# Kernel tuning notes

Hardware: AMD Instinct MI355X
Metric: run time of the kernel (lower is better)

Reference implementation:

```python
import jax, jax.numpy as jnp
import numpy as np

N_NODES = 50000
N_EDGES = 800000
IN_DIM = 64
HID_DIM = 64
OUT_DIM = 16
N_RELS = 16
N_BASES = 4


def setup_inputs() -> dict:
    key = jax.random.key(0)
    ks = jax.random.split(key, 11)
    feats = jax.random.normal(ks[0], (N_NODES, IN_DIM), dtype=jnp.float32)
    src = jax.random.randint(ks[1], (N_EDGES,), 0, N_NODES, dtype=jnp.int32)
    dst = jax.random.randint(ks[2], (N_EDGES,), 0, N_NODES, dtype=jnp.int32)
    edge_type = jax.random.randint(ks[3], (N_EDGES,), 0, N_RELS, dtype=jnp.int32)
    edge_norm = jax.random.uniform(ks[4], (N_EDGES,), dtype=jnp.float32)
    # basis-decomposed relation weights: W[r] = sum_b coef[r,b] * bases[b]
    bases1 = jax.random.normal(ks[5], (N_BASES, IN_DIM, HID_DIM), dtype=jnp.float32) * (1.0 / np.sqrt(IN_DIM))
    coef1 = jax.random.normal(ks[6], (N_RELS, N_BASES), dtype=jnp.float32)
    bias1 = jnp.zeros((HID_DIM,), dtype=jnp.float32)
    bases2 = jax.random.normal(ks[7], (N_BASES, HID_DIM, OUT_DIM), dtype=jnp.float32) * (1.0 / np.sqrt(HID_DIM))
    coef2 = jax.random.normal(ks[8], (N_RELS, N_BASES), dtype=jnp.float32)
    bias2 = jnp.zeros((OUT_DIM,), dtype=jnp.float32)
    return {"feats": feats, "src": src, "dst": dst, "edge_type": edge_type,
            "edge_norm": edge_norm, "bases1": bases1, "coef1": coef1, "bias1": bias1,
            "bases2": bases2, "coef2": coef2, "bias2": bias2}


def _rel_graph_conv(x, src, dst, edge_type, edge_norm, bases, coef, bias):
    """One RelGraphConv layer (basis decomposition, low-mem: gather coef, not W)."""
    xs = x[src]                                   # [E, in]  gather source feats
    t = jnp.einsum('ei,bio->ebo', xs, bases)      # [E, B, out] per-basis transform
    c = coef[edge_type]                            # [E, B]   per-edge relation coefs
    msg = jnp.einsum('eb,ebo->eo', c, t)          # [E, out]
    msg = msg * edge_norm[:, None]                # apply edge norm
    h = jax.ops.segment_sum(msg, dst, num_segments=N_NODES)  # scatter-add by dst
    return jax.nn.relu(h + bias)                  # bias + activation (dropout=0, eval)


def reference(feats, src, dst, edge_type, edge_norm, bases1, coef1, bias1, bases2, coef2, bias2):
    h = _rel_graph_conv(feats, src, dst, edge_type, edge_norm, bases1, coef1, bias1)
    h = _rel_graph_conv(h, src, dst, edge_type, edge_norm, bases2, coef2, bias2)
    return h
```

## Files before the change

### kernel.cpp

```cpp
#include <hip/hip_runtime.h>

#define N_NODES 50000
#define N_EDGES 800000

typedef __attribute__((ext_vector_type(8))) short bf16x8;
typedef __attribute__((ext_vector_type(4))) float f32x4;

__device__ __forceinline__ unsigned bf16rne(float x) {
  unsigned u = __float_as_uint(x);
  return (u + 0x7FFFu + ((u >> 16) & 1u)) >> 16;
}
__device__ __forceinline__ unsigned packbf2(float a, float b) {
  return bf16rne(a) | (bf16rne(b) << 16);
}
__device__ __forceinline__ float bflo(unsigned u) { return __uint_as_float(u << 16); }
__device__ __forceinline__ float bfhi(unsigned u) { return __uint_as_float(u & 0xFFFF0000u); }

__global__ __launch_bounds__(256) void k_pack(
    const float4* __restrict__ feats4, uint2* __restrict__ xbf,
    const float* __restrict__ bases1, const float* __restrict__ bases2,
    unsigned short* __restrict__ b1T, unsigned short* __restrict__ b2p) {
  if (blockIdx.x < 3125) {
    const int i = blockIdx.x * 256 + threadIdx.x;
    float4 v = feats4[i];
    xbf[i] = make_uint2(packbf2(v.x, v.y), packbf2(v.z, v.w));
  } else {
    for (int idx = threadIdx.x; idx < 64 * 256; idx += 256) {
      int o = idx >> 8, q = idx & 255;
      b1T[idx] = (unsigned short)bf16rne(bases1[q * 64 + o]);
    }
    for (int idx = threadIdx.x; idx < 64 * 64; idx += 256) {
      int j = idx >> 6, k = idx & 63;
      int o = j >> 2, b = j & 3;
      b2p[idx] = (unsigned short)bf16rne(bases2[b * 1024 + k * 16 + o]);
    }
  }
}

#define G_HIST 64
#define CHUNK (N_EDGES / G_HIST)
#define NSLICE 4
#define HBINS (N_NODES / NSLICE)

__global__ __launch_bounds__(512) void k_hist(
    const int* __restrict__ dst, unsigned char* __restrict__ rank,
    unsigned short* __restrict__ bh) {
  __shared__ int hist[HBINS];
  const int c = blockIdx.x & (G_HIST - 1);
  const int p = blockIdx.x >> 6;
  const int e0 = c * CHUNK;
  const int lo = p * HBINS;
  for (int i = threadIdx.x; i < HBINS; i += 512) hist[i] = 0;
  __syncthreads();
  for (int i = threadIdx.x; i < CHUNK; i += 512) {
    const int d = dst[e0 + i] - lo;
    if ((unsigned)d < (unsigned)HBINS)
      rank[e0 + i] = (unsigned char)atomicAdd(&hist[d], 1);
  }
  __syncthreads();
  for (int i = threadIdx.x; i < HBINS; i += 512)
    bh[(size_t)c * N_NODES + lo + i] = (unsigned short)hist[i];
}

#define NB 512
__global__ __launch_bounds__(512) void k_scan1(
    unsigned short* __restrict__ bh,
    int* __restrict__ rowp, int* __restrict__ bsum) {
  __shared__ unsigned short tile[G_HIST][NB];
  __shared__ int wsum[8];
  const int tid = threadIdx.x;
  const int n0 = blockIdx.x * NB;
  for (int idx = tid; idx < G_HIST * (NB / 4); idx += 512) {
    const int c = idx >> 7, j = idx & 127;
    const int nloc = 4 * j;
    uint2 u = make_uint2(0u, 0u);
    if (n0 + nloc < N_NODES)
      u = *(const uint2*)(bh + (size_t)c * N_NODES + n0 + nloc);
    *(uint2*)&tile[c][nloc] = u;
  }
  __syncthreads();
  int s = 0;
  for (int c = 0; c < G_HIST; ++c) {
    const int cnt = tile[c][tid];
    tile[c][tid] = (unsigned short)s;
    s += cnt;
  }
  __syncthreads();
  for (int idx = tid; idx < G_HIST * (NB / 4); idx += 512) {
    const int c = idx >> 7, j = idx & 127;
    const int nloc = 4 * j;
    if (n0 + nloc < N_NODES)
      *(uint2*)(bh + (size_t)c * N_NODES + n0 + nloc) = *(uint2*)&tile[c][nloc];
  }
  const int lane = tid & 63, wid = tid >> 6;
  int v = (n0 + tid < N_NODES) ? s : 0;
  int incl = v;
#pragma unroll
  for (int off = 1; off < 64; off <<= 1) {
    int t = __shfl_up(incl, off, 64);
    if (lane >= off) incl += t;
  }
  if (lane == 63) wsum[wid] = incl;
  __syncthreads();
  if (tid < 8) {
    int wi = wsum[tid];
#pragma unroll
    for (int off = 1; off < 8; off <<= 1) {
      int t = __shfl_up(wi, off, 64);
      if (lane >= off) wi += t;
    }
    wsum[tid] = wi;
  }
  __syncthreads();
  int woff = (wid > 0) ? wsum[wid - 1] : 0;
  int incl_all = incl + woff;
  if (n0 + tid < N_NODES) rowp[n0 + tid + 1] = incl_all;
  if (tid == NB - 1) bsum[blockIdx.x] = incl_all;
}

__global__ __launch_bounds__(512) void k_scan3(int* __restrict__ rowp,
                                               const int* __restrict__ bsum) {
  __shared__ int s_off;
  const int tid = threadIdx.x;
  if (tid < 64) {
    int v = 0;
    for (int b = tid; b < (int)blockIdx.x; b += 64) v += bsum[b];
#pragma unroll
    for (int off = 32; off >= 1; off >>= 1) v += __shfl_down(v, off, 64);
    if (tid == 0) s_off = v;
  }
  __syncthreads();
  const int i = blockIdx.x * NB + tid;
  if (i < N_NODES) rowp[i + 1] += s_off;
  if (i == 0) rowp[0] = 0;
}

__global__ __launch_bounds__(256) void k_scatter(
    const int* __restrict__ src, const int* __restrict__ dst,
    const int* __restrict__ ety, const float* __restrict__ enorm,
    const int* __restrict__ rowp, const unsigned char* __restrict__ rank,
    const unsigned short* __restrict__ bh, unsigned* __restrict__ s_edge) {
  int e = blockIdx.x * 256 + threadIdx.x;
  if (e >= N_EDGES) return;
  const int d = dst[e];
  const int b = e / CHUNK;
  const int pos = rowp[d] + (int)bh[(size_t)b * N_NODES + d] + (int)rank[e];
  unsigned nq = (unsigned)(enorm[e] * 4096.f + 0.5f);
  nq = nq > 4095u ? 4095u : nq;
  s_edge[pos] = (unsigned)src[e] | ((unsigned)ety[e] << 16) | (nq << 20);
}

#define NMSCALE (1.f / 4096.f)

#define ROWB 264
__device__ __forceinline__ void gather_node(
    const int* __restrict__ rowp, const unsigned* __restrict__ s_edge,
    const uint2* __restrict__ xv, const float4* __restrict__ coefLDS,
    unsigned short* __restrict__ uA,
    int node, int m, int lane) {
  const int eslot = lane >> 4, ch4 = lane & 15;
  const int beg = rowp[node], end = rowp[node + 1];
  const int qlen = (end - beg + 3) >> 2;
  int p = beg + eslot * qlen;
  const int pend = min(p + qlen, end);
  float4 a0 = {0, 0, 0, 0}, a1 = {0, 0, 0, 0}, a2 = {0, 0, 0, 0}, a3 = {0, 0, 0, 0};
  for (; p < pend; p += 4) {
    const int nb = pend - p;
    unsigned rec[4];
#pragma unroll
    for (int t = 0; t < 4; ++t) rec[t] = (t < nb) ? s_edge[p + t] : 0u;
    uint2 xp[4];
#pragma unroll
    for (int t = 0; t < 4; ++t) xp[t] = xv[(rec[t] & 0xFFFF) * 16 + ch4];
#pragma unroll
    for (int t = 0; t < 4; ++t) {
      const float nm = (float)(rec[t] >> 20) * NMSCALE;
      const float4 c = coefLDS[(rec[t] >> 16) & 15];
      const float w0 = nm * c.x, w1 = nm * c.y, w2 = nm * c.z, w3 = nm * c.w;
      const float x0 = bflo(xp[t].x), x1 = bfhi(xp[t].x);
      const float x2 = bflo(xp[t].y), x3 = bfhi(xp[t].y);
      a0.x += w0 * x0; a0.y += w0 * x1; a0.z += w0 * x2; a0.w += w0 * x3;
      a1.x += w1 * x0; a1.y += w1 * x1; a1.z += w1 * x2; a1.w += w1 * x3;
      a2.x += w2 * x0; a2.y += w2 * x1; a2.z += w2 * x2; a2.w += w2 * x3;
      a3.x += w3 * x0; a3.y += w3 * x1; a3.z += w3 * x2; a3.w += w3 * x3;
    }
  }
#define RED1(x) x += __shfl_down(x, 32, 64)
  RED1(a0.x); RED1(a0.y); RED1(a0.z); RED1(a0.w);
  RED1(a1.x); RED1(a1.y); RED1(a1.z); RED1(a1.w);
  RED1(a2.x); RED1(a2.y); RED1(a2.z); RED1(a2.w);
  RED1(a3.x); RED1(a3.y); RED1(a3.z); RED1(a3.w);
#undef RED1
  if (eslot < 2) {
    unsigned short* row = uA + (eslot * 16 + m) * ROWB + 4 * ch4;
    *(uint2*)(row + 0 * 64) = make_uint2(packbf2(a0.x, a0.y), packbf2(a0.z, a0.w));
    *(uint2*)(row + 1 * 64) = make_uint2(packbf2(a1.x, a1.y), packbf2(a1.z, a1.w));
    *(uint2*)(row + 2 * 64) = make_uint2(packbf2(a2.x, a2.y), packbf2(a2.z, a2.w));
    *(uint2*)(row + 3 * 64) = make_uint2(packbf2(a3.x, a3.y), packbf2(a3.z, a3.w));
  }
}

__global__ __launch_bounds__(256) void k_l1_fused(
    const int* __restrict__ rowp, const unsigned* __restrict__ s_edge,
    const uint2* __restrict__ xbf, const float* __restrict__ coef1,
    const unsigned short* __restrict__ b1T,
    const float* __restrict__ bias1,
    const unsigned short* __restrict__ b2p,
    uint2* __restrict__ y2bf) {
  __shared__ __align__(16) unsigned short uA[2 * 16 * ROWB];
  __shared__ float coefs[64];
  __shared__ float cmat[16 * 68];
  const int wid = threadIdx.x >> 6, lane = threadIdx.x & 63;
  if (threadIdx.x < 64) coefs[threadIdx.x] = coef1[threadIdx.x];
  __syncthreads();
  const int nbase = blockIdx.x * 16;
#pragma unroll
  for (int jn = 0; jn < 4; ++jn) {
    const int m = wid * 4 + jn;
    gather_node(rowp, s_edge, xbf, (const float4*)coefs, uA, nbase + m, m, lane);
  }
  __syncthreads();
  const int nloc = lane & 15, kgrp = lane >> 4;
  f32x4 acc1 = {0.f, 0.f, 0.f, 0.f};
#pragma unroll
  for (int ks = 0; ks < 8; ++ks) {
    const int k0 = ks * 32 + kgrp * 8;
    const bf16x8 b = *(const bf16x8*)&b1T[(wid * 16 + nloc) * 256 + k0];
    const bf16x8 aS0 = *(const bf16x8*)&uA[(0 * 16 + nloc) * ROWB + k0];
    acc1 = __builtin_amdgcn_mfma_f32_16x16x32_bf16(aS0, b, acc1, 0, 0, 0);
    const bf16x8 aS1 = *(const bf16x8*)&uA[(1 * 16 + nloc) * ROWB + k0];
    acc1 = __builtin_amdgcn_mfma_f32_16x16x32_bf16(aS1, b, acc1, 0, 0, 0);
  }
  {
    const int o = wid * 16 + nloc;
    const float bs = bias1[o];
#pragma unroll
    for (int r = 0; r < 4; ++r) {
      const int m = (lane >> 4) * 4 + r;
      cmat[m * 68 + o] = fmaxf(acc1[r] + bs, 0.f);
    }
  }
  __syncthreads();
  f32x4 acc2 = {0.f, 0.f, 0.f, 0.f};
#pragma unroll
  for (int ks = 0; ks < 2; ++ks) {
    const int k0 = ks * 32 + kgrp * 8;
    const float4 c0 = *(const float4*)&cmat[nloc * 68 + k0];
    const float4 c1 = *(const float4*)&cmat[nloc * 68 + k0 + 4];
    union { bf16x8 v; unsigned u[4]; } au;
    au.u[0] = packbf2(c0.x, c0.y); au.u[1] = packbf2(c0.z, c0.w);
    au.u[2] = packbf2(c1.x, c1.y); au.u[3] = packbf2(c1.z, c1.w);
    const bf16x8 b = *(const bf16x8*)&b2p[(wid * 16 + nloc) * 64 + k0];
    acc2 = __builtin_amdgcn_mfma_f32_16x16x32_bf16(au.v, b, acc2, 0, 0, 0);
  }
  __syncthreads();
#pragma unroll
  for (int r = 0; r < 4; ++r) {
    const int m = (lane >> 4) * 4 + r;
    cmat[m * 68 + wid * 16 + nloc] = acc2[r];
  }
  __syncthreads();
  const int nl = threadIdx.x >> 4, c4 = threadIdx.x & 15;
  const float* cr = &cmat[nl * 68 + 4 * c4];
  y2bf[(size_t)(nbase + nl) * 16 + c4] =
      make_uint2(packbf2(cr[0], cr[1]), packbf2(cr[2], cr[3]));
}

__global__ __launch_bounds__(256) void k_l2_gather(
    const int* __restrict__ rowp, const unsigned* __restrict__ s_edge,
    const uint4* __restrict__ y2v,
    const float* __restrict__ coef2, const float* __restrict__ bias2,
    float2* __restrict__ out) {
  __shared__ float coefs[64];
  if (threadIdx.x < 64) coefs[threadIdx.x] = coef2[threadIdx.x];
  __syncthreads();
  const float4* coefv = (const float4*)coefs;
  const int wid = threadIdx.x >> 6, lane = threadIdx.x & 63;
  const int eslot = lane >> 3, og = lane & 7;
  const int nbase = blockIdx.x * 8 + wid * 2;

  float a0[2] = {0.f, 0.f}, a1[2] = {0.f, 0.f};
  int p[2], pend[2];
#pragma unroll
  for (int m = 0; m < 2; ++m) {
    const int beg = rowp[nbase + m], end = rowp[nbase + m + 1];
    const int qlen = (end - beg + 7) >> 3;
    p[m] = beg + eslot * qlen;
    pend[m] = min(p[m] + qlen, end);
  }
  while ((p[0] < pend[0]) | (p[1] < pend[1])) {
    unsigned rec[2][2] = {{0u, 0u}, {0u, 0u}};
#pragma unroll
    for (int m = 0; m < 2; ++m) {
      if (p[m] < pend[m]) rec[m][0] = s_edge[p[m]];
      if (p[m] + 1 < pend[m]) rec[m][1] = s_edge[p[m] + 1];
    }
    uint4 yp[2][2];
#pragma unroll
    for (int m = 0; m < 2; ++m)
#pragma unroll
      for (int t = 0; t < 2; ++t)
        yp[m][t] = y2v[(rec[m][t] & 0xFFFF) * 8 + og];
#pragma unroll
    for (int m = 0; m < 2; ++m)
#pragma unroll
      for (int t = 0; t < 2; ++t) {
        const float nm = (float)(rec[m][t] >> 20) * NMSCALE;
        const float4 c = coefv[(rec[m][t] >> 16) & 15];
        a0[m] += nm * (c.x * bflo(yp[m][t].x) + c.y * bfhi(yp[m][t].x) +
                       c.z * bflo(yp[m][t].y) + c.w * bfhi(yp[m][t].y));
        a1[m] += nm * (c.x * bflo(yp[m][t].z) + c.y * bfhi(yp[m][t].z) +
                       c.z * bflo(yp[m][t].w) + c.w * bfhi(yp[m][t].w));
      }
#pragma unroll
    for (int m = 0; m < 2; ++m) p[m] += 2;
  }
#pragma unroll
  for (int m = 0; m < 2; ++m) {
    a0[m] += __shfl_down(a0[m], 32, 64);
    a0[m] += __shfl_down(a0[m], 16, 64);
    a0[m] += __shfl_down(a0[m], 8, 64);
    a1[m] += __shfl_down(a1[m], 32, 64);
    a1[m] += __shfl_down(a1[m], 16, 64);
    a1[m] += __shfl_down(a1[m], 8, 64);
  }
  if (eslot == 0) {
    const float b0 = bias2[2 * og], b1 = bias2[2 * og + 1];
#pragma unroll
    for (int m = 0; m < 2; ++m) {
      out[(size_t)(nbase + m) * 8 + og] =
          make_float2(fmaxf(a0[m] + b0, 0.f), fmaxf(a1[m] + b1, 0.f));
    }
  }
}

extern "C" void kernel_launch(void* const* d_in, const int* in_sizes, int n_in,
                              void* d_out, int out_size, void* d_ws, size_t ws_size,
                              hipStream_t stream) {
  const float* feats  = (const float*)d_in[0];
  const int*   src    = (const int*)d_in[1];
  const int*   dst    = (const int*)d_in[2];
  const int*   etype  = (const int*)d_in[3];
  const float* enorm  = (const float*)d_in[4];
  const float* bases1 = (const float*)d_in[5];
  const float* coef1  = (const float*)d_in[6];
  const float* bias1  = (const float*)d_in[7];
  const float* bases2 = (const float*)d_in[8];
  const float* coef2  = (const float*)d_in[9];
  const float* bias2  = (const float*)d_in[10];

  uint2* xbf    = (uint2*)d_ws;
  uint2* y2bf   = xbf + (size_t)N_NODES * 16;
  unsigned* s_edge = (unsigned*)(y2bf + (size_t)N_NODES * 16);
  unsigned short* bh = (unsigned short*)(s_edge + N_EDGES);
  unsigned short* b1T = bh + (size_t)G_HIST * N_NODES;
  unsigned short* b2p = b1T + 64 * 256;
  int*   rowp   = (int*)(b2p + 64 * 64);
  int*   bsum   = rowp + N_NODES + 1;
  unsigned char* rank = (unsigned char*)(bsum + 128);

  const int SCAN_BLKS = (N_NODES + NB - 1) / NB;

  k_pack<<<3126, 256, 0, stream>>>((const float4*)feats, xbf, bases1,
                                   bases2, b1T, b2p);
  k_hist<<<G_HIST * NSLICE, 512, 0, stream>>>(dst, rank, bh);
  k_scan1<<<SCAN_BLKS, 512, 0, stream>>>(bh, rowp, bsum);
  k_scan3<<<SCAN_BLKS, 512, 0, stream>>>(rowp, bsum);
  k_scatter<<<N_EDGES / 256, 256, 0, stream>>>(src, dst, etype, enorm,
                                               rowp, rank, bh, s_edge);
  k_l1_fused<<<N_NODES / 16, 256, 0, stream>>>(rowp, s_edge, xbf, coef1,
                                               b1T, bias1, b2p, y2bf);
  k_l2_gather<<<N_NODES / 8, 256, 0, stream>>>(rowp, s_edge,
                                               (const uint4*)y2bf, coef2,
                                               bias2, (float2*)d_out);
}
```

Before: 191.8 us.

## Fuse pack with histogram and fold block-offset scan into consumers

Merges the feature/basis packing kernel with the destination histogram kernel into one launch. It also drops the separate scan-fixup kernel: rowp now holds block-local exclusive prefixes, and scatter, layer-1 and layer-2 kernels each reconstruct global offsets from bsum. This removes two kernel launches and a pass over rowp. In exchange, every scatter block redundantly scans 128 block sums and the gather kernels do a small strided reduction.

Result: faster. 186.6 us, median of 2 (-2.8%).

```diff
diff --git a/kernel.cpp b/kernel.cpp
--- a/kernel.cpp
+++ b/kernel.cpp
@@ -15,54 +15,58 @@
 }
 __device__ __forceinline__ float bflo(unsigned u) { return __uint_as_float(u << 16); }
 __device__ __forceinline__ float bfhi(unsigned u) { return __uint_as_float(u & 0xFFFF0000u); }
-
-__global__ __launch_bounds__(256) void k_pack(
-    const float4* __restrict__ feats4, uint2* __restrict__ xbf,
-    const float* __restrict__ bases1, const float* __restrict__ bases2,
-    unsigned short* __restrict__ b1T, unsigned short* __restrict__ b2p) {
-  if (blockIdx.x < 3125) {
-    const int i = blockIdx.x * 256 + threadIdx.x;
-    float4 v = feats4[i];
-    xbf[i] = make_uint2(packbf2(v.x, v.y), packbf2(v.z, v.w));
-  } else {
-    for (int idx = threadIdx.x; idx < 64 * 256; idx += 256) {
-      int o = idx >> 8, q = idx & 255;
-      b1T[idx] = (unsigned short)bf16rne(bases1[q * 64 + o]);
-    }
-    for (int idx = threadIdx.x; idx < 64 * 64; idx += 256) {
-      int j = idx >> 6, k = idx & 63;
-      int o = j >> 2, b = j & 3;
-      b2p[idx] = (unsigned short)bf16rne(bases2[b * 1024 + k * 16 + o]);
-    }
-  }
-}
 
 #define G_HIST 64
 #define CHUNK (N_EDGES / G_HIST)
 #define NSLICE 4
 #define HBINS (N_NODES / NSLICE)
-
-__global__ __launch_bounds__(512) void k_hist(
+#define NB 512
+#define SCAN_BLKS ((N_NODES + NB - 1) / NB)
+#define NHIST (G_HIST * NSLICE)
+#define NPACK ((N_EDGES + 511) / 512)
+
+__global__ __launch_bounds__(512) void k_prep(
+    const float4* __restrict__ feats4, uint2* __restrict__ xbf,
+    const float* __restrict__ bases1, const float* __restrict__ bases2,
+    unsigned short* __restrict__ b1T, unsigned short* __restrict__ b2p,
     const int* __restrict__ dst, unsigned char* __restrict__ rank,
     unsigned short* __restrict__ bh) {
   __shared__ int hist[HBINS];
-  const int c = blockIdx.x & (G_HIST - 1);
-  const int p = blockIdx.x >> 6;
-  const int e0 = c * CHUNK;
-  const int lo = p * HBINS;
-  for (int i = threadIdx.x; i < HBINS; i += 512) hist[i] = 0;
-  __syncthreads();
-  for (int i = threadIdx.x; i < CHUNK; i += 512) {
-    const int d = dst[e0 + i] - lo;
-    if ((unsigned)d < (unsigned)HBINS)
-      rank[e0 + i] = (unsigned char)atomicAdd(&hist[d], 1);
-  }
-  __syncthreads();
-  for (int i = threadIdx.x; i < HBINS; i += 512)
-    bh[(size_t)c * N_NODES + lo + i] = (unsigned short)hist[i];
-}
-
-#define NB 512
+  const int bid = blockIdx.x;
+  if (bid < NHIST) {
+    const int c = bid & (G_HIST - 1);
+    const int p = bid >> 6;
+    const int e0 = c * CHUNK;
+    const int lo = p * HBINS;
+    for (int i = threadIdx.x; i < HBINS; i += 512) hist[i] = 0;
+    __syncthreads();
+    for (int i = threadIdx.x; i < CHUNK; i += 512) {
+      const int d = dst[e0 + i] - lo;
+      if ((unsigned)d < (unsigned)HBINS)
+        rank[e0 + i] = (unsigned char)atomicAdd(&hist[d], 1);
+    }
+    __syncthreads();
+    for (int i = threadIdx.x; i < HBINS; i += 512)
+      bh[(size_t)c * N_NODES + lo + i] = (unsigned short)hist[i];
+  } else if (bid < NHIST + NPACK) {
+    const int i = (bid - NHIST) * 512 + threadIdx.x;
+    if (i < N_EDGES) {
+      float4 v = feats4[i];
+      xbf[i] = make_uint2(packbf2(v.x, v.y), packbf2(v.z, v.w));
+    }
+  } else {
+    for (int idx = threadIdx.x; idx < 64 * 256; idx += 512) {
+      int o = idx >> 8, q = idx & 255;
+      b1T[idx] = (unsigned short)bf16rne(bases1[q * 64 + o]);
+    }
+    for (int idx = threadIdx.x; idx < 64 * 64; idx += 512) {
+      int j = idx >> 6, k = idx & 63;
+      int o = j >> 2, b = j & 3;
+      b2p[idx] = (unsigned short)bf16rne(bases2[b * 1024 + k * 16 + o]);
+    }
+  }
+}
+
 __global__ __launch_bounds__(512) void k_scan1(
     unsigned short* __restrict__ bh,
     int* __restrict__ rowp, int* __restrict__ bsum) {
@@ -93,7 +97,7 @@
       *(uint2*)(bh + (size_t)c * N_NODES + n0 + nloc) = *(uint2*)&tile[c][nloc];
   }
   const int lane = tid & 63, wid = tid >> 6;
-  int v = (n0 + tid < N_NODES) ? s : 0;
+  const int v = (n0 + tid < N_NODES) ? s : 0;
   int incl = v;
 #pragma unroll
   for (int off = 1; off < 64; off <<= 1) {
@@ -112,39 +116,47 @@
     wsum[tid] = wi;
   }
   __syncthreads();
-  int woff = (wid > 0) ? wsum[wid - 1] : 0;
-  int incl_all = incl + woff;
-  if (n0 + tid < N_NODES) rowp[n0 + tid + 1] = incl_all;
+  const int woff = (wid > 0) ? wsum[wid - 1] : 0;
+  const int incl_all = incl + woff;
+  const int n = n0 + tid;
+  if (n <= N_NODES) rowp[n] = incl_all - v;
   if (tid == NB - 1) bsum[blockIdx.x] = incl_all;
 }
 
-__global__ __launch_bounds__(512) void k_scan3(int* __restrict__ rowp,
-                                               const int* __restrict__ bsum) {
-  __shared__ int s_off;
-  const int tid = threadIdx.x;
-  if (tid < 64) {
-    int v = 0;
-    for (int b = tid; b < (int)blockIdx.x; b += 64) v += bsum[b];
-#pragma unroll
-    for (int off = 32; off >= 1; off >>= 1) v += __shfl_down(v, off, 64);
-    if (tid == 0) s_off = v;
-  }
-  __syncthreads();
-  const int i = blockIdx.x * NB + tid;
-  if (i < N_NODES) rowp[i + 1] += s_off;
-  if (i == 0) rowp[0] = 0;
+__device__ __forceinline__ int prefix_bsum(const int* __restrict__ bsum,
+                                           int b, int lane) {
+  int v = 0;
+  for (int k = lane; k < b; k += 64) v += bsum[k];
+#pragma unroll
+  for (int off = 32; off >= 1; off >>= 1) v += __shfl_xor(v, off, 64);
+  return v;
 }
 
 __global__ __launch_bounds__(256) void k_scatter(
     const int* __restrict__ src, const int* __restrict__ dst,
     const int* __restrict__ ety, const float* __restrict__ enorm,
     const int* __restrict__ rowp, const unsigned char* __restrict__ rank,
-    const unsigned short* __restrict__ bh, unsigned* __restrict__ s_edge) {
-  int e = blockIdx.x * 256 + threadIdx.x;
+    const unsigned short* __restrict__ bh, const int* __restrict__ bsum,
+    unsigned* __restrict__ s_edge) {
+  __shared__ int sb[128];
+  const int tid = threadIdx.x;
+  if (tid < 128) sb[tid] = (tid < SCAN_BLKS) ? bsum[tid] : 0;
+  __syncthreads();
+#pragma unroll
+  for (int off = 1; off < 128; off <<= 1) {
+    int t = 0;
+    if (tid < 128 && tid >= off) t = sb[tid - off];
+    __syncthreads();
+    if (tid < 128) sb[tid] += t;
+    __syncthreads();
+  }
+  const int e = blockIdx.x * 256 + tid;
   if (e >= N_EDGES) return;
   const int d = dst[e];
   const int b = e / CHUNK;
-  const int pos = rowp[d] + (int)bh[(size_t)b * N_NODES + d] + (int)rank[e];
+  const int blk = d >> 9;
+  const int boff = blk ? sb[blk - 1] : 0;
+  const int pos = rowp[d] + boff + (int)bh[(size_t)b * N_NODES + d] + (int)rank[e];
   unsigned nq = (unsigned)(enorm[e] * 4096.f + 0.5f);
   nq = nq > 4095u ? 4095u : nq;
   s_edge[pos] = (unsigned)src[e] | ((unsigned)ety[e] << 16) | (nq << 20);
@@ -154,12 +166,11 @@
 
 #define ROWB 264
 __device__ __forceinline__ void gather_node(
-    const int* __restrict__ rowp, const unsigned* __restrict__ s_edge,
-    const uint2* __restrict__ xv, const float4* __restrict__ coefLDS,
+    const unsigned* __restrict__ s_edge, const uint2* __restrict__ xv,
+    const float4* __restrict__ coefLDS,
     unsigned short* __restrict__ uA,
-    int node, int m, int lane) {
+    int beg, int end, int m, int lane) {
   const int eslot = lane >> 4, ch4 = lane & 15;
-  const int beg = rowp[node], end = rowp[node + 1];
   const int qlen = (end - beg + 3) >> 2;
   int p = beg + eslot * qlen;
   const int pend = min(p + qlen, end);
@@ -201,7 +212,8 @@
 }
 
 __global__ __launch_bounds__(256) void k_l1_fused(
-    const int* __restrict__ rowp, const unsigned* __restrict__ s_edge,
+    const int* __restrict__ rowp, const int* __restrict__ bsum,
+    const unsigned* __restrict__ s_edge,
     const uint2* __restrict__ xbf, const float* __restrict__ coef1,
     const unsigned short* __restrict__ b1T,
     const float* __restrict__ bias1,
@@ -214,10 +226,16 @@
   if (threadIdx.x < 64) coefs[threadIdx.x] = coef1[threadIdx.x];
   __syncthreads();
   const int nbase = blockIdx.x * 16;
+  const int b0 = nbase >> 9;
+  const int boff0 = prefix_bsum(bsum, b0, lane);
+  const int bs0 = bsum[b0];
 #pragma unroll
   for (int jn = 0; jn < 4; ++jn) {
     const int m = wid * 4 + jn;
-    gather_node(rowp, s_edge, xbf, (const float4*)coefs, uA, nbase + m, m, lane);
+    const int node = nbase + m;
+    const int beg = rowp[node] + (((node >> 9) == b0) ? boff0 : boff0 + bs0);
+    const int end = rowp[node + 1] + ((((node + 1) >> 9) == b0) ? boff0 : boff0 + bs0);
+    gather_node(s_edge, xbf, (const float4*)coefs, uA, beg, end, m, lane);
   }
   __syncthreads();
   const int nloc = lane & 15, kgrp = lane >> 4;
@@ -267,7 +285,8 @@
 }
 
 __global__ __launch_bounds__(256) void k_l2_gather(
-    const int* __restrict__ rowp, const unsigned* __restrict__ s_edge,
+    const int* __restrict__ rowp, const int* __restrict__ bsum,
+    const unsigned* __restrict__ s_edge,
     const uint4* __restrict__ y2v,
     const float* __restrict__ coef2, const float* __restrict__ bias2,
     float2* __restrict__ out) {
@@ -278,12 +297,17 @@
   const int wid = threadIdx.x >> 6, lane = threadIdx.x & 63;
   const int eslot = lane >> 3, og = lane & 7;
   const int nbase = blockIdx.x * 8 + wid * 2;
+  const int b0 = nbase >> 9;
+  const int boff0 = prefix_bsum(bsum, b0, lane);
+  const int bs0 = bsum[b0];
 
   float a0[2] = {0.f, 0.f}, a1[2] = {0.f, 0.f};
   int p[2], pend[2];
 #pragma unroll
   for (int m = 0; m < 2; ++m) {
-    const int beg = rowp[nbase + m], end = rowp[nbase + m + 1];
+    const int node = nbase + m;
+    const int beg = rowp[node] + (((node >> 9) == b0) ? boff0 : boff0 + bs0);
+    const int end = rowp[node + 1] + ((((node + 1) >> 9) == b0) ? boff0 : boff0 + bs0);
     const int qlen = (end - beg + 7) >> 3;
     p[m] = beg + eslot * qlen;
     pend[m] = min(p[m] + qlen, end);
@@ -325,11 +349,11 @@
     a1[m] += __shfl_down(a1[m], 8, 64);
   }
   if (eslot == 0) {
-    const float b0 = bias2[2 * og], b1 = bias2[2 * og + 1];
+    const float b0s = bias2[2 * og], b1s = bias2[2 * og + 1];
 #pragma unroll
     for (int m = 0; m < 2; ++m) {
       out[(size_t)(nbase + m) * 8 + og] =
-          make_float2(fmaxf(a0[m] + b0, 0.f), fmaxf(a1[m] + b1, 0.f));
+          make_float2(fmaxf(a0[m] + b0s, 0.f), fmaxf(a1[m] + b1s, 0.f));
     }
   }
 }
@@ -359,18 +383,14 @@
   int*   bsum   = rowp + N_NODES + 1;
   unsigned char* rank = (unsigned char*)(bsum + 128);
 
-  const int SCAN_BLKS = (N_NODES + NB - 1) / NB;
-
-  k_pack<<<3126, 256, 0, stream>>>((const float4*)feats, xbf, bases1,
-                                   bases2, b1T, b2p);
-  k_hist<<<G_HIST * NSLICE, 512, 0, stream>>>(dst, rank, bh);
+  k_prep<<<NHIST + NPACK + 1, 512, 0, stream>>>(
+      (const float4*)feats, xbf, bases1, bases2, b1T, b2p, dst, rank, bh);
   k_scan1<<<SCAN_BLKS, 512, 0, stream>>>(bh, rowp, bsum);
-  k_scan3<<<SCAN_BLKS, 512, 0, stream>>>(rowp, bsum);
-  k_scatter<<<N_EDGES / 256, 256, 0, stream>>>(src, dst, etype, enorm,
-                                               rowp, rank, bh, s_edge);
-  k_l1_fused<<<N_NODES / 16, 256, 0, stream>>>(rowp, s_edge, xbf, coef1,
+  k_scatter<<<(N_EDGES + 255) / 256, 256, 0, stream>>>(
+      src, dst, etype, enorm, rowp, rank, bh, bsum, s_edge);
+  k_l1_fused<<<N_NODES / 16, 256, 0, stream>>>(rowp, bsum, s_edge, xbf, coef1,
                                                b1T, bias1, b2p, y2bf);
-  k_l2_gather<<<N_NODES / 8, 256, 0, stream>>>(rowp, s_edge,
+  k_l2_gather<<<N_NODES / 8, 256, 0, stream>>>(rowp, bsum, s_edge,
                                                (const uint4*)y2bf, coef2,
                                                bias2, (float2*)d_out);
 }
```
